# Kernel optimization log

Hardware: AMD Instinct MI355X
Metric: run time of the kernel (lower is better)

## Reference

```python
import jax, jax.numpy as jnp
import numpy as np
from jax import lax

TIMESTEPS = 10
KSIZE = 2
STRIDE = 2


def setup_inputs() -> dict:
    key = jax.random.key(0)
    k1, _ = jax.random.split(key)
    x = jax.random.normal(k1, (32, 96, 128, 128), dtype=jnp.float32)
    # torch init: np.full((1, C, 1, 1), 0.1)
    pool_strength = jnp.ones((1, 96, 1, 1), dtype=jnp.float32) * 0.1
    return {"x": x, "pool_strength": pool_strength}


def _maxpool3x3_same(x):
    # MaxPool2d(kernel=3, stride=1, padding=1) on NCHW
    return lax.reduce_window(
        x, -jnp.inf, lax.max,
        window_dimensions=(1, 1, 3, 3),
        window_strides=(1, 1, 1, 1),
        padding=((0, 0), (0, 0), (1, 1), (1, 1)))


def reference(x, pool_strength):
    def step(cur, _):
        pooled = _maxpool3x3_same(cur)
        cur = cur + pool_strength * (pooled - cur)
        return cur, None

    cur, _ = lax.scan(step, x, None, length=TIMESTEPS)
    # AvgPool2d(kernel=2, stride=2, padding=0)
    s = lax.reduce_window(
        cur, 0.0, lax.add,
        window_dimensions=(1, 1, KSIZE, KSIZE),
        window_strides=(1, 1, STRIDE, STRIDE),
        padding='VALID')
    return s / float(KSIZE * KSIZE)
```

## Files before the change

### kernel.cpp

```cpp
#include <hip/hip_runtime.h>


#define TSTEPS 10
#define PW 128
#define HP 132
#define HROWS 31

__device__ __forceinline__ float dpp_left(float x) {
    int r = __builtin_amdgcn_update_dpp((int)0xff800000, __float_as_int(x),
                                        0x111, 0xf, 0xf, false);
    return __int_as_float(r);
}
__device__ __forceinline__ float dpp_right(float x) {
    int r = __builtin_amdgcn_update_dpp((int)0xff800000, __float_as_int(x),
                                        0x101, 0xf, 0xf, false);
    return __int_as_float(r);
}

__device__ __forceinline__ float max3f(float a, float b, float c) {
    return fmaxf(fmaxf(a, b), c);
}

__device__ __forceinline__ void hmax_row(const float* v, float* h) {
    float vl = dpp_left(v[7]);
    float vr = dpp_right(v[0]);
    h[0] = max3f(vl, v[0], v[1]);
#pragma unroll
    for (int c = 1; c < 7; ++c) h[c] = max3f(v[c - 1], v[c], v[c + 1]);
    h[7] = max3f(v[6], v[7], vr);
}

__device__ __forceinline__ void ld8(const float* a, float* d) {
    float4 u = ((const float4*)a)[0], v = ((const float4*)a)[1];
    d[0] = u.x; d[1] = u.y; d[2] = u.z; d[3] = u.w;
    d[4] = v.x; d[5] = v.y; d[6] = v.z; d[7] = v.w;
}
__device__ __forceinline__ void st8(float* a, const float* d) {
    ((float4*)a)[0] = make_float4(d[0], d[1], d[2], d[3]);
    ((float4*)a)[1] = make_float4(d[4], d[5], d[6], d[7]);
}

__device__ __forceinline__ void do_step(float cur[4][8], float p, int tx, int ty,
                                        float* __restrict__ topBuf,
                                        float* __restrict__ botBuf) {
    const float NEG = -__builtin_huge_valf();
    const int x0 = tx * 8;

    float hTop[8], hBot[8];
    hmax_row(cur[0], hTop);
    hmax_row(cur[3], hBot);

    if (ty > 0)  st8(topBuf + (ty - 1) * HP + x0, hTop);
    if (ty < 31) st8(botBuf + ty * HP + x0, hBot);

    __syncthreads();

    float hm[8], hnx[8];
    if (ty > 0) {
        ld8(botBuf + (ty - 1) * HP + x0, hm);
    } else {
#pragma unroll
        for (int c = 0; c < 8; ++c) hm[c] = NEG;
    }
    if (ty < 31) {
        ld8(topBuf + ty * HP + x0, hnx);
    } else {
#pragma unroll
        for (int c = 0; c < 8; ++c) hnx[c] = NEG;
    }

    float hc[8];
#pragma unroll
    for (int c = 0; c < 8; ++c) hc[c] = hTop[c];

#pragma unroll
    for (int r = 0; r < 4; ++r) {
        float hn[8];
        if (r < 2) {
            hmax_row(cur[r + 1], hn);
        } else if (r == 2) {
#pragma unroll
            for (int c = 0; c < 8; ++c) hn[c] = hBot[c];
        } else {
#pragma unroll
            for (int c = 0; c < 8; ++c) hn[c] = hnx[c];
        }
#pragma unroll
        for (int c = 0; c < 8; ++c) {
            float v = max3f(hm[c], hc[c], hn[c]);
            cur[r][c] = fmaf(p, v - cur[r][c], cur[r][c]);
        }
#pragma unroll
        for (int c = 0; c < 8; ++c) { hm[c] = hc[c]; hc[c] = hn[c]; }
    }
}

__global__ __launch_bounds__(512, 4)
void cpool_kernel(const float* __restrict__ x, const float* __restrict__ ps,
                  float* __restrict__ out) {
    __shared__ float lds[2][2][HROWS * HP];

    const int b = blockIdx.x;
    const float p = ps[b % 96];

    const int tx = threadIdx.x & 15;
    const int ty = threadIdx.x >> 4;
    const int x0 = tx * 8;
    const int y0 = ty * 4;

    const float* __restrict__ xp = x + (size_t)b * (PW * PW);

    float cur[4][8];
#pragma unroll
    for (int r = 0; r < 4; ++r) ld8(xp + (y0 + r) * PW + x0, cur[r]);

#pragma unroll 1
    for (int tt = 0; tt < TSTEPS / 2; ++tt) {
        do_step(cur, p, tx, ty, lds[0][0], lds[0][1]);
        do_step(cur, p, tx, ty, lds[1][0], lds[1][1]);
    }

    float* __restrict__ op = out + (size_t)b * (64 * 64);
#pragma unroll
    for (int r2 = 0; r2 < 2; ++r2) {
        float4 o;
        o.x = 0.25f * (cur[2*r2][0] + cur[2*r2][1] + cur[2*r2+1][0] + cur[2*r2+1][1]);
        o.y = 0.25f * (cur[2*r2][2] + cur[2*r2][3] + cur[2*r2+1][2] + cur[2*r2+1][3]);
        o.z = 0.25f * (cur[2*r2][4] + cur[2*r2][5] + cur[2*r2+1][4] + cur[2*r2+1][5]);
        o.w = 0.25f * (cur[2*r2][6] + cur[2*r2][7] + cur[2*r2+1][6] + cur[2*r2+1][7]);
        *(float4*)(op + (size_t)((2 * ty + r2) * 64 + tx * 4)) = o;
    }
}

extern "C" void kernel_launch(void* const* d_in, const int* in_sizes, int n_in,
                              void* d_out, int out_size, void* d_ws, size_t ws_size,
                              hipStream_t stream) {
    const float* x  = (const float*)d_in[0];
    const float* ps = (const float*)d_in[1];
    float* out = (float*)d_out;
    (void)in_sizes; (void)n_in; (void)out_size; (void)d_ws; (void)ws_size;

    cpool_kernel<<<dim3(32 * 96), dim3(512), 0, stream>>>(x, ps, out);
}
```

Baseline: 292.9 us.

## Give each thread an 8x8 tile and halve block size to 256

Each thread now holds 8 rows by 8 columns of the plane in registers instead of 4x8, and the block shrinks to 256 threads (16 row-groups). Halo row exchange through LDS is needed only at 15 boundaries instead of 31, so the LDS traffic and the horizontal-max recomputation per output row go down. The cost is more registers per thread (64 state floats plus temporaries), which may limit occupancy or cause spills, and fewer waves are available to hide barrier latency.

New measurement: 480.5 us. +64.1%, slower.

```diff
diff --git a/kernel.cpp b/kernel.cpp
--- a/kernel.cpp
+++ b/kernel.cpp
@@ -4,7 +4,6 @@
 #define TSTEPS 10
 #define PW 128
 #define HP 132
-#define HROWS 31
 
 __device__ __forceinline__ float dpp_left(float x) {
     int r = __builtin_amdgcn_update_dpp((int)0xff800000, __float_as_int(x),
@@ -40,7 +39,7 @@
     ((float4*)a)[1] = make_float4(d[4], d[5], d[6], d[7]);
 }
 
-__device__ __forceinline__ void do_step(float cur[4][8], float p, int tx, int ty,
+__device__ __forceinline__ void do_step(float cur[8][8], float p, int tx, int ty,
                                         float* __restrict__ topBuf,
                                         float* __restrict__ botBuf) {
     const float NEG = -__builtin_huge_valf();
@@ -48,57 +47,63 @@
 
     float hTop[8], hBot[8];
     hmax_row(cur[0], hTop);
-    hmax_row(cur[3], hBot);
-
+    hmax_row(cur[7], hBot);
     if (ty > 0)  st8(topBuf + (ty - 1) * HP + x0, hTop);
-    if (ty < 31) st8(botBuf + ty * HP + x0, hBot);
+    if (ty < 15) st8(botBuf + ty * HP + x0, hBot);
 
     __syncthreads();
 
-    float hm[8], hnx[8];
+    float hmE[8], hnE[8];
     if (ty > 0) {
-        ld8(botBuf + (ty - 1) * HP + x0, hm);
+        ld8(botBuf + (ty - 1) * HP + x0, hmE);
     } else {
 #pragma unroll
-        for (int c = 0; c < 8; ++c) hm[c] = NEG;
+        for (int c = 0; c < 8; ++c) hmE[c] = NEG;
     }
-    if (ty < 31) {
-        ld8(topBuf + ty * HP + x0, hnx);
+    if (ty < 15) {
+        ld8(topBuf + ty * HP + x0, hnE);
     } else {
 #pragma unroll
-        for (int c = 0; c < 8; ++c) hnx[c] = NEG;
+        for (int c = 0; c < 8; ++c) hnE[c] = NEG;
     }
 
-    float hc[8];
+    float A[8], B[8];
+    hmax_row(cur[1], B);
 #pragma unroll
-    for (int c = 0; c < 8; ++c) hc[c] = hTop[c];
+    for (int c = 0; c < 8; ++c) {
+        float v = max3f(hmE[c], hTop[c], B[c]);
+        cur[0][c] = fmaf(p, v - cur[0][c], cur[0][c]);
+        A[c] = hTop[c];
+    }
 
 #pragma unroll
-    for (int r = 0; r < 4; ++r) {
-        float hn[8];
-        if (r < 2) {
-            hmax_row(cur[r + 1], hn);
-        } else if (r == 2) {
-#pragma unroll
-            for (int c = 0; c < 8; ++c) hn[c] = hBot[c];
+    for (int r = 1; r < 7; ++r) {
+        float C[8];
+        if (r < 6) {
+            hmax_row(cur[r + 1], C);
         } else {
 #pragma unroll
-            for (int c = 0; c < 8; ++c) hn[c] = hnx[c];
+            for (int c = 0; c < 8; ++c) C[c] = hBot[c];
         }
 #pragma unroll
         for (int c = 0; c < 8; ++c) {
-            float v = max3f(hm[c], hc[c], hn[c]);
+            float v = max3f(A[c], B[c], C[c]);
             cur[r][c] = fmaf(p, v - cur[r][c], cur[r][c]);
+            A[c] = B[c]; B[c] = C[c];
         }
+    }
+
 #pragma unroll
-        for (int c = 0; c < 8; ++c) { hm[c] = hc[c]; hc[c] = hn[c]; }
+    for (int c = 0; c < 8; ++c) {
+        float v = max3f(A[c], B[c], hnE[c]);
+        cur[7][c] = fmaf(p, v - cur[7][c], cur[7][c]);
     }
 }
 
-__global__ __launch_bounds__(512, 4)
+__global__ __launch_bounds__(256, 4)
 void cpool_kernel(const float* __restrict__ x, const float* __restrict__ ps,
                   float* __restrict__ out) {
-    __shared__ float lds[2][2][HROWS * HP];
+    __shared__ float lds[2][2][15 * HP];
 
     const int b = blockIdx.x;
     const float p = ps[b % 96];
@@ -106,13 +111,13 @@
     const int tx = threadIdx.x & 15;
     const int ty = threadIdx.x >> 4;
     const int x0 = tx * 8;
-    const int y0 = ty * 4;
+    const int y0 = ty * 8;
 
     const float* __restrict__ xp = x + (size_t)b * (PW * PW);
 
-    float cur[4][8];
+    float cur[8][8];
 #pragma unroll
-    for (int r = 0; r < 4; ++r) ld8(xp + (y0 + r) * PW + x0, cur[r]);
+    for (int r = 0; r < 8; ++r) ld8(xp + (y0 + r) * PW + x0, cur[r]);
 
 #pragma unroll 1
     for (int tt = 0; tt < TSTEPS / 2; ++tt) {
@@ -122,13 +127,13 @@
 
     float* __restrict__ op = out + (size_t)b * (64 * 64);
 #pragma unroll
-    for (int r2 = 0; r2 < 2; ++r2) {
+    for (int r2 = 0; r2 < 4; ++r2) {
         float4 o;
         o.x = 0.25f * (cur[2*r2][0] + cur[2*r2][1] + cur[2*r2+1][0] + cur[2*r2+1][1]);
         o.y = 0.25f * (cur[2*r2][2] + cur[2*r2][3] + cur[2*r2+1][2] + cur[2*r2+1][3]);
         o.z = 0.25f * (cur[2*r2][4] + cur[2*r2][5] + cur[2*r2+1][4] + cur[2*r2+1][5]);
         o.w = 0.25f * (cur[2*r2][6] + cur[2*r2][7] + cur[2*r2+1][6] + cur[2*r2+1][7]);
-        *(float4*)(op + (size_t)((2 * ty + r2) * 64 + tx * 4)) = o;
+        *(float4*)(op + (size_t)((ty * 4 + r2) * 64 + tx * 4)) = o;
     }
 }
 
@@ -140,5 +145,5 @@
     float* out = (float*)d_out;
     (void)in_sizes; (void)n_in; (void)out_size; (void)d_ws; (void)ws_size;
 
-    cpool_kernel<<<dim3(32 * 96), dim3(512), 0, stream>>>(x, ps, out);
+    cpool_kernel<<<dim3(32 * 96), dim3(256), 0, stream>>>(x, ps, out);
 }
```
